# Kernel optimization log

Measured on AMD Instinct MI355X. Metric: run time of the kernel, lower is better.

The kernel has to match this reference:

```python
import jax, jax.numpy as jnp
import numpy as np

B, DV, DT, H, G, E = 4096, 1024, 1024, 1024, 4096, 8
D = DV + DT  # fused dim = 2048


def setup_inputs() -> dict:
    key = jax.random.key(0)
    ks = jax.random.split(key, 8)
    s = 0.02
    return {
        "vision_cls": jax.random.normal(ks[0], (B, DV), jnp.float32),
        "text_cls": jax.random.normal(ks[1], (B, DT), jnp.float32),
        "W1_imm": jax.random.normal(ks[2], (E, D, H), jnp.float32) * s,
        "b1_imm": jnp.zeros((E, H), jnp.float32),
        "W2_imm": jax.random.normal(ks[3], (E, H, 1), jnp.float32) * s,
        "b2_imm": jnp.zeros((E, 1), jnp.float32),
        "W1_gene": jax.random.normal(ks[4], (E, D, H), jnp.float32) * s,
        "b1_gene": jnp.zeros((E, H), jnp.float32),
        "W2_gene": jax.random.normal(ks[5], (E, H, G), jnp.float32) * s,
        "b2_gene": jnp.zeros((E, G), jnp.float32),
        "organ_idx": jax.random.randint(ks[6], (B,), 0, E, jnp.int32),
    }


def reference(vision_cls, text_cls, W1_imm, b1_imm, W2_imm, b2_imm,
              W1_gene, b1_gene, W2_gene, b2_gene, organ_idx):
    # fused features [B, D]
    fused = jnp.concatenate([vision_cls, text_cls], axis=-1)
    # Dense MoE reference: run every organ head on the full batch, then
    # select each sample's routed output (same math as the per-group
    # gather -> MLP -> scatter in the original; dropout is eval-mode identity).
    h_i = jax.nn.relu(jnp.einsum('bd,edh->ebh', fused, W1_imm) + b1_imm[:, None, :])
    imm_all = jnp.einsum('ebh,eh->eb', h_i, W2_imm[:, :, 0]) + b2_imm[:, :1]  # [E,B]
    h_g = jax.nn.relu(jnp.einsum('bd,edh->ebh', fused, W1_gene) + b1_gene[:, None, :])
    gene_all = jnp.einsum('ebh,ehg->ebg', h_g, W2_gene) + b2_gene[:, None, :]  # [E,B,G]
    bidx = jnp.arange(fused.shape[0])
    immune = imm_all[organ_idx, bidx]      # [B]
    gene = gene_all[organ_idx, bidx]       # [B,G] (uniform gene_dim -> no padding needed)
    return immune, gene, vision_cls, text_cls
```

## Files before the change

### kernel.cpp

```cpp
#include <hip/hip_runtime.h>


#define B_N 4096
#define DV  1024
#define DD  2048
#define HH  1024
#define GG  4096
#define EE  8
#define BM  128
#define MAXRB 40
#define PERM_N (MAXRB * BM)

typedef __bf16 bf16x8 __attribute__((ext_vector_type(8)));
typedef float f32x4 __attribute__((ext_vector_type(4)));
typedef unsigned short u16x4v __attribute__((ext_vector_type(4)));
typedef unsigned short u16x8v __attribute__((ext_vector_type(8)));

#define H_CNT 0
#define H_FIL 8
#define H_OFF 16
#define H_NRB 24
#define H_BLK 32

static __device__ __forceinline__ unsigned short f2bf(float f) {
  return __builtin_bit_cast(unsigned short, (__bf16)f);
}
static __device__ __forceinline__ float bf2f(unsigned short s) {
  return __builtin_bit_cast(float, (unsigned)s << 16);
}
static __device__ __forceinline__ void gload16(const void* g, void* l) {
  __builtin_amdgcn_global_load_lds(
      (const __attribute__((address_space(1))) unsigned int*)g,
      (__attribute__((address_space(3))) unsigned int*)l, 16, 0, 0);
}

__global__ __launch_bounds__(1024) void routing(const int* __restrict__ organ,
                                                int* __restrict__ hdr,
                                                int* __restrict__ perm) {
  __shared__ int cnt[EE], fil[EE], off[EE];
  const int tid = threadIdx.x;
  if (tid < EE) { cnt[tid] = 0; fil[tid] = 0; }
  __syncthreads();
#pragma unroll
  for (int i = 0; i < 4; ++i) atomicAdd(&cnt[organ[tid + (i << 10)]], 1);
#pragma unroll
  for (int i = 0; i < 5; ++i) perm[tid + (i << 10)] = -1;
  __syncthreads();
  if (tid == 0) {
    int acc = 0;
    for (int e = 0; e < EE; ++e) {
      off[e] = acc;
      hdr[H_OFF + e] = acc;
      hdr[H_CNT + e] = cnt[e];
      int nb = (cnt[e] + BM - 1) >> 7;
      int rb0 = acc >> 7;
      for (int i = 0; i < nb; ++i) hdr[H_BLK + rb0 + i] = e;
      acc += nb << 7;
    }
    hdr[H_NRB] = acc >> 7;
  }
  __syncthreads();
#pragma unroll
  for (int i = 0; i < 4; ++i) {
    int b = tid + (i << 10);
    int e = organ[b];
    int slot = off[e] + atomicAdd(&fil[e], 1);
    perm[slot] = b;
  }
}

__global__ __launch_bounds__(256) void k_A(
    const float* __restrict__ vis, const float* __restrict__ txt,
    const int* __restrict__ hdr, const int* __restrict__ perm,
    unsigned short* __restrict__ Abuf) {
  const int bx = blockIdx.x;
  const int nr = hdr[H_NRB] << 7;
  const int tid = threadIdx.x;
  const int c = tid << 3;
  const float* srcbase = (c < DV) ? vis : txt;
  const int cc = (c < DV) ? c : c - DV;
#pragma unroll
  for (int p = 0; p < 4; ++p) {
    int r = (bx << 2) + p;
    if (r >= nr) return;
    int smp = perm[r];
    u16x8v v;
    if (smp >= 0) {
      const float* src = srcbase + (size_t)smp * 1024 + cc;
      float4 a = *(const float4*)src, b = *(const float4*)(src + 4);
      v[0] = f2bf(a.x); v[1] = f2bf(a.y); v[2] = f2bf(a.z); v[3] = f2bf(a.w);
      v[4] = f2bf(b.x); v[5] = f2bf(b.y); v[6] = f2bf(b.z); v[7] = f2bf(b.w);
    } else {
#pragma unroll
      for (int i = 0; i < 8; ++i) v[i] = 0;
    }
    *(u16x8v*)&Abuf[(size_t)r * DD + c] = v;
  }
}

static __device__ __forceinline__ void copy_body(
    int bx, const float4* __restrict__ v, const float4* __restrict__ t,
    float4* __restrict__ ov, float4* __restrict__ ot) {
  const int n4 = B_N * DV / 4;
  for (int i = bx * 256 + (int)threadIdx.x; i < n4; i += 1024 * 256) {
    ov[i] = v[i];
    ot[i] = t[i];
  }
}

template <int KDIM, int NST>
static __device__ __forceinline__ void gemm_core(
    const unsigned short* __restrict__ Aseg,
    const float* __restrict__ Bglob,
    unsigned short* smem, f32x4 (&acc)[4][4]) {
  const int tid = threadIdx.x;
  const int lane = tid & 63;
  const int wr = ((tid >> 6) >> 1) << 6, wc = ((tid >> 6) & 1) << 6;
  const int lr = lane & 15;
  const int arow = tid >> 2;
  const int kq_src = (((tid & 3) ^ ((arow >> 1) & 3)) << 3);
  const int wbase = (tid & 192) << 3;
  const int bn4 = (tid & 31) << 2;
  const int bk4 = (tid >> 5) << 2;
  constexpr int NT = KDIM / 32;

  float4 bvE[4], bvO[4];

  auto issueA = [&](int buf, int k0) {
    unsigned short* d = smem + (buf << 12) + wbase;
    gload16(Aseg + (size_t)arow * KDIM + k0 + kq_src, d);
    gload16(Aseg + (size_t)(64 + arow) * KDIM + k0 + kq_src, d + 2048);
  };
  auto issueB = [&](float4 (&bv)[4], int k0) {
    const float* p = Bglob + (size_t)(k0 + bk4) * NST + bn4;
#pragma unroll
    for (int i = 0; i < 4; ++i) bv[i] = *(const float4*)(p + (size_t)i * NST);
  };
  auto writeB = [&](int buf, float4 (&bv)[4]) {
    const float* f0 = (const float*)&bv[0];
    const float* f1 = (const float*)&bv[1];
    const float* f2 = (const float*)&bv[2];
    const float* f3 = (const float*)&bv[3];
#pragma unroll
    for (int j = 0; j < 4; ++j) {
      const int n = bn4 + j;
      const int s3 = (n ^ (n >> 3)) & 7;
      u16x4v w;
      w[0] = f2bf(f0[j]); w[1] = f2bf(f1[j]);
      w[2] = f2bf(f2[j]); w[3] = f2bf(f3[j]);
      *(u16x4v*)(smem + 16384 + (buf << 12) + (n << 5) + ((((bk4 >> 2)) ^ s3) << 2)) = w;
    }
  };
  auto compute = [&](int ab, int bb) {
    bf16x8 af[4], bfr[4];
#pragma unroll
    for (int m = 0; m < 4; ++m) {
      const int r = wr + m * 16 + lr;
      const int cs = ((lane >> 4) ^ ((r >> 1) & 3)) << 3;
      af[m] = *(const bf16x8*)&smem[(ab << 12) + r * 32 + cs];
    }
#pragma unroll
    for (int n = 0; n < 4; ++n) {
      const int fr = wc + n * 16 + lr;
      const int s3 = (fr ^ (fr >> 3)) & 7;
      const unsigned short* row = smem + 16384 + (bb << 12) + (fr << 5);
      const int g = (lane >> 4) << 1;
      union { unsigned long long q[2]; bf16x8 v; } u;
      u.q[0] = *(const unsigned long long*)(row + ((g ^ s3) << 2));
      u.q[1] = *(const unsigned long long*)(row + (((g + 1) ^ s3) << 2));
      bfr[n] = u.v;
    }
#pragma unroll
    for (int m = 0; m < 4; ++m)
#pragma unroll
      for (int n = 0; n < 4; ++n)
        acc[m][n] = __builtin_amdgcn_mfma_f32_16x16x32_bf16(af[m], bfr[n], acc[m][n], 0, 0, 0);
  };

  auto phase = [&](int t, float4 (&bvIss)[4], float4 (&bvWr)[4]) {
    if (t + 3 < NT) issueA((t + 3) & 3, (t + 3) << 5);
    __builtin_amdgcn_sched_barrier(0);
    if (t + 2 < NT) issueB(bvIss, (t + 2) << 5);
    __builtin_amdgcn_sched_barrier(0);
    compute(t & 3, t & 1);
    if (t + 1 < NT) writeB((t + 1) & 1, bvWr);
    asm volatile("s_waitcnt lgkmcnt(0)" ::: "memory");
    __builtin_amdgcn_s_barrier();
    __builtin_amdgcn_sched_barrier(0);
  };

  issueA(0, 0);
  __builtin_amdgcn_sched_barrier(0);
  issueB(bvE, 0);
  writeB(0, bvE);
  issueA(1, 1 << 5);
  __builtin_amdgcn_sched_barrier(0);
  issueA(2, 2 << 5);
  __builtin_amdgcn_sched_barrier(0);
  issueB(bvO, 1 << 5);
  asm volatile("s_waitcnt lgkmcnt(0)" ::: "memory");
  __builtin_amdgcn_s_barrier();
  __builtin_amdgcn_sched_barrier(0);

  for (int t = 0; t < NT; t += 2) {
    phase(t, bvE, bvO);
    phase(t + 1, bvO, bvE);
  }
}

#define G_L1 (MAXRB * 16)
__global__ __launch_bounds__(256) void k_L1(
    const unsigned short* __restrict__ Abuf, const float* __restrict__ W1i,
    const float* __restrict__ W1g, const float* __restrict__ b1i,
    const float* __restrict__ b1g, const int* __restrict__ hdr,
    unsigned short* __restrict__ H1, unsigned short* __restrict__ H2,
    const float4* __restrict__ vis4, const float4* __restrict__ txt4,
    float4* __restrict__ ov, float4* __restrict__ ot) {
  __shared__ __align__(16) unsigned short smem[24576];
  int bx = blockIdx.x;
  if (bx >= G_L1) { copy_body(bx - G_L1, vis4, txt4, ov, ot); return; }
  const int id = (bx & 7) * (G_L1 >> 3) + (bx >> 3);
  const int rb = id % MAXRB;
  if (rb >= hdr[H_NRB]) return;
  const int sub = id / MAXRB, head = sub >> 3, cb = (sub & 7) << 7;
  const int e = hdr[H_BLK + rb];
  const float* Bglob = (head ? W1g : W1i) + (size_t)e * DD * HH + cb;
  const float* bias = (head ? b1g : b1i) + e * HH;
  unsigned short* Hout = head ? H2 : H1;
  const int tid = threadIdx.x;
  const int lane = tid & 63, wave = tid >> 6;
  const int wr = (wave >> 1) << 6, wc = (wave & 1) << 6;
  const int lr = lane & 15;

  f32x4 acc[4][4];
#pragma unroll
  for (int m = 0; m < 4; ++m)
#pragma unroll
    for (int n = 0; n < 4; ++n) acc[m][n] = (f32x4){0.f, 0.f, 0.f, 0.f};

  gemm_core<DD, HH>(Abuf + (size_t)rb * BM * DD, Bglob, smem, acc);
  __syncthreads();

  const int r0l = wr + ((lane >> 4) << 2);
#pragma unroll
  for (int n = 0; n < 4; ++n) {
    const int col = wc + n * 16 + lr;
    const float bv = bias[cb + col];
#pragma unroll
    for (int m = 0; m < 4; ++m)
#pragma unroll
      for (int v = 0; v < 4; ++v) {
        int row = r0l + m * 16 + v;
        float x = acc[m][n][v] + bv;
        x = x > 0.f ? x : 0.f;
        smem[((row << 7) + col) ^ ((row & 7) << 3)] = f2bf(x);
      }
  }
  __syncthreads();
#pragma unroll
  for (int c = 0; c < 8; ++c) {
    int q = c * 256 + tid;
    int row = q >> 4, ch = q & 15;
    int off = ((row << 7) + (ch << 3)) ^ ((row & 7) << 3);
    u16x8v val = *(const u16x8v*)&smem[off];
    *(u16x8v*)&Hout[(size_t)(rb * BM + row) * HH + cb + (ch << 3)] = val;
  }
}

static __device__ __forceinline__ void immune_body(
    int bx, const int* __restrict__ hdr, const int* __restrict__ perm,
    const unsigned short* __restrict__ H1, const float* __restrict__ W2,
    const float* __restrict__ b2, float* __restrict__ out) {
  const int nrb = hdr[H_NRB];
  const int r = bx * 4 + (threadIdx.x >> 6);
  if (r >= nrb * BM) return;
  const int b = perm[r];
  if (b < 0) return;
  const int e = hdr[H_BLK + (r >> 7)];
  const int lane = threadIdx.x & 63;
  const unsigned short* h = H1 + (size_t)r * HH + lane * 16;
  const float* w = W2 + (size_t)e * HH + lane * 16;
  float s = 0.f;
#pragma unroll
  for (int i = 0; i < 16; ++i) s += bf2f(h[i]) * w[i];
#pragma unroll
  for (int off = 32; off >= 1; off >>= 1) s += __shfl_xor(s, off, 64);
  if (lane == 0) out[b] = s + b2[e];
}

#define G_L2 (MAXRB * 32)
__global__ __launch_bounds__(256) void k_L2(
    const unsigned short* __restrict__ H2buf, const float* __restrict__ W2g,
    const float* __restrict__ b2g, const int* __restrict__ hdr,
    const int* __restrict__ perm, float* __restrict__ outg,
    const unsigned short* __restrict__ H1, const float* __restrict__ W2i,
    const float* __restrict__ b2i, float* __restrict__ outi) {
  __shared__ __align__(16) unsigned short smem[24576];
  int bx = blockIdx.x;
  if (bx >= G_L2) {
    immune_body(bx - G_L2, hdr, perm, H1, W2i, b2i, outi);
    return;
  }
  const int id = (bx & 7) * (G_L2 >> 3) + (bx >> 3);
  const int rb = id % MAXRB;
  if (rb >= hdr[H_NRB]) return;
  const int cb = (id / MAXRB) << 7;
  const int e = hdr[H_BLK + rb];
  const float* Bglob = W2g + (size_t)e * HH * GG + cb;
  const int tid = threadIdx.x;
  const int lane = tid & 63, wave = tid >> 6;
  const int wr = (wave >> 1) << 6, wc = (wave & 1) << 6;
  const int lr = lane & 15;

  f32x4 acc[4][4];
#pragma unroll
  for (int m = 0; m < 4; ++m)
#pragma unroll
    for (int n = 0; n < 4; ++n) acc[m][n] = (f32x4){0.f, 0.f, 0.f, 0.f};

  gemm_core<HH, GG>(H2buf + (size_t)rb * BM * HH, Bglob, smem, acc);
  __syncthreads();

  const int r0l = wr + ((lane >> 4) << 2);
#pragma unroll
  for (int n = 0; n < 4; ++n) {
    const int col = wc + n * 16 + lr;
    const float bv = b2g[e * GG + cb + col];
#pragma unroll
    for (int m = 0; m < 4; ++m)
#pragma unroll
      for (int v = 0; v < 4; ++v) {
        int row = r0l + m * 16 + v;
        smem[((row << 7) + col) ^ ((row & 7) << 3)] = f2bf(acc[m][n][v] + bv);
      }
  }
  __syncthreads();
#pragma unroll
  for (int c = 0; c < 8; ++c) {
    int q = c * 256 + tid;
    int row = q >> 4, ch = q & 15;
    int sm = perm[rb * BM + row];
    if (sm < 0) continue;
    int off = ((row << 7) + (ch << 3)) ^ ((row & 7) << 3);
    u16x8v val = *(const u16x8v*)&smem[off];
    float4 f0, f1;
    f0.x = bf2f(val[0]); f0.y = bf2f(val[1]); f0.z = bf2f(val[2]); f0.w = bf2f(val[3]);
    f1.x = bf2f(val[4]); f1.y = bf2f(val[5]); f1.z = bf2f(val[6]); f1.w = bf2f(val[7]);
    float* dst = outg + (size_t)sm * GG + cb + (ch << 3);
    *(float4*)dst = f0;
    *(float4*)(dst + 4) = f1;
  }
}

extern "C" void kernel_launch(void* const* d_in, const int* in_sizes, int n_in,
                              void* d_out, int out_size, void* d_ws, size_t ws_size,
                              hipStream_t stream) {
  (void)in_sizes; (void)n_in; (void)out_size; (void)ws_size;
  const float* vis = (const float*)d_in[0];
  const float* txt = (const float*)d_in[1];
  const float* W1i = (const float*)d_in[2];
  const float* b1i = (const float*)d_in[3];
  const float* W2i = (const float*)d_in[4];
  const float* b2i = (const float*)d_in[5];
  const float* W1g = (const float*)d_in[6];
  const float* b1g = (const float*)d_in[7];
  const float* W2g = (const float*)d_in[8];
  const float* b2g = (const float*)d_in[9];
  const int* organ = (const int*)d_in[10];

  float* out_imm = (float*)d_out;
  float* out_gene = out_imm + B_N;
  float* out_vis = out_gene + (size_t)B_N * GG;
  float* out_txt = out_vis + (size_t)B_N * DV;

  int* hdr = (int*)d_ws;
  int* perm = hdr + 128;

  const size_t OFF_ABUF = 32768;
  const size_t OFF_H1 = OFF_ABUF + (size_t)PERM_N * DD * 2;
  const size_t OFF_H2 = OFF_H1 + (size_t)PERM_N * HH * 2;
  unsigned short* Abuf = (unsigned short*)((char*)d_ws + OFF_ABUF);
  unsigned short* H1 = (unsigned short*)((char*)d_ws + OFF_H1);
  unsigned short* H2 = (unsigned short*)((char*)d_ws + OFF_H2);

  routing<<<1, 1024, 0, stream>>>(organ, hdr, perm);
  k_A<<<PERM_N / 4, 256, 0, stream>>>(vis, txt, hdr, perm, Abuf);
  k_L1<<<G_L1 + 1024, 256, 0, stream>>>(Abuf, W1i, W1g, b1i, b1g, hdr, H1, H2,
                                        (const float4*)vis, (const float4*)txt,
                                        (float4*)out_vis, (float4*)out_txt);
  k_L2<<<G_L2 + PERM_N / 4, 256, 0, stream>>>(H2, W2g, b2g, hdr, perm, out_gene,
                                              H1, W2i, b2i, out_imm);
}
```

Baseline: 250.3 us.

## Shrink A-buffer ring to three stages and halve L1 tile width

```diff
diff --git a/kernel.cpp b/kernel.cpp
--- a/kernel.cpp
+++ b/kernel.cpp
@@ -108,62 +108,74 @@
   }
 }
 
-template <int KDIM, int NST>
-static __device__ __forceinline__ void gemm_core(
+template <int KDIM, int NST, int NB>
+static __device__ __forceinline__ void gemm_core3(
     const unsigned short* __restrict__ Aseg,
     const float* __restrict__ Bglob,
-    unsigned short* smem, f32x4 (&acc)[4][4]) {
+    unsigned short* smem, f32x4 (&acc)[4][NB]) {
   const int tid = threadIdx.x;
   const int lane = tid & 63;
-  const int wr = ((tid >> 6) >> 1) << 6, wc = ((tid >> 6) & 1) << 6;
+  const int wr = ((tid >> 6) >> 1) << 6;
+  const int wc = ((tid >> 6) & 1) * (NB * 16);
   const int lr = lane & 15;
   const int arow = tid >> 2;
   const int kq_src = (((tid & 3) ^ ((arow >> 1) & 3)) << 3);
   const int wbase = (tid & 192) << 3;
-  const int bn4 = (tid & 31) << 2;
-  const int bk4 = (tid >> 5) << 2;
+  const int cg = tid & (8 * NB - 1);
+  const int bn4 = cg << 2;
+  const int kr = (tid / (8 * NB)) * NB;
   constexpr int NT = KDIM / 32;
-
-  float4 bvE[4], bvO[4];
-
-  auto issueA = [&](int buf, int k0) {
-    unsigned short* d = smem + (buf << 12) + wbase;
+  constexpr int BSZ = NB * 32 * 32;
+  const int s3w = (bn4 ^ (bn4 >> 3)) & 7;
+
+  float4 bvE[NB], bvO[NB];
+  (void)s3w;
+
+  auto issueA = [&](int ab, int k0) {
+    unsigned short* d = smem + ab * 4096 + wbase;
     gload16(Aseg + (size_t)arow * KDIM + k0 + kq_src, d);
     gload16(Aseg + (size_t)(64 + arow) * KDIM + k0 + kq_src, d + 2048);
   };
-  auto issueB = [&](float4 (&bv)[4], int k0) {
-    const float* p = Bglob + (size_t)(k0 + bk4) * NST + bn4;
-#pragma unroll
-    for (int i = 0; i < 4; ++i) bv[i] = *(const float4*)(p + (size_t)i * NST);
+  auto issueB = [&](float4 (&bv)[NB], int k0) {
+    const float* p = Bglob + (size_t)(k0 + kr) * NST + bn4;
+#pragma unroll
+    for (int i = 0; i < NB; ++i) bv[i] = *(const float4*)(p + (size_t)i * NST);
   };
-  auto writeB = [&](int buf, float4 (&bv)[4]) {
-    const float* f0 = (const float*)&bv[0];
-    const float* f1 = (const float*)&bv[1];
-    const float* f2 = (const float*)&bv[2];
-    const float* f3 = (const float*)&bv[3];
+  auto writeB = [&](int bb, float4 (&bv)[NB]) {
+    unsigned short* base = smem + 12288 + bb * BSZ;
 #pragma unroll
     for (int j = 0; j < 4; ++j) {
       const int n = bn4 + j;
       const int s3 = (n ^ (n >> 3)) & 7;
-      u16x4v w;
-      w[0] = f2bf(f0[j]); w[1] = f2bf(f1[j]);
-      w[2] = f2bf(f2[j]); w[3] = f2bf(f3[j]);
-      *(u16x4v*)(smem + 16384 + (buf << 12) + (n << 5) + ((((bk4 >> 2)) ^ s3) << 2)) = w;
+      unsigned short* row = base + (n << 5);
+      if constexpr (NB == 4) {
+        u16x4v w;
+        w[0] = f2bf(((const float*)&bv[0])[j]);
+        w[1] = f2bf(((const float*)&bv[1])[j]);
+        w[2] = f2bf(((const float*)&bv[2])[j]);
+        w[3] = f2bf(((const float*)&bv[3])[j]);
+        *(u16x4v*)(row + (((kr >> 2) ^ s3) << 2)) = w;
+      } else {
+        unsigned lo = f2bf(((const float*)&bv[0])[j]);
+        unsigned hi = f2bf(((const float*)&bv[1])[j]);
+        *(unsigned*)(row + ((((kr >> 2) ^ s3) << 2) | (kr & 2))) =
+            lo | (hi << 16);
+      }
     }
   };
   auto compute = [&](int ab, int bb) {
-    bf16x8 af[4], bfr[4];
+    bf16x8 af[4], bfr[NB];
 #pragma unroll
     for (int m = 0; m < 4; ++m) {
       const int r = wr + m * 16 + lr;
       const int cs = ((lane >> 4) ^ ((r >> 1) & 3)) << 3;
-      af[m] = *(const bf16x8*)&smem[(ab << 12) + r * 32 + cs];
+      af[m] = *(const bf16x8*)&smem[ab * 4096 + r * 32 + cs];
     }
 #pragma unroll
-    for (int n = 0; n < 4; ++n) {
+    for (int n = 0; n < NB; ++n) {
       const int fr = wc + n * 16 + lr;
       const int s3 = (fr ^ (fr >> 3)) & 7;
-      const unsigned short* row = smem + 16384 + (bb << 12) + (fr << 5);
+      const unsigned short* row = smem + 12288 + bb * BSZ + (fr << 5);
       const int g = (lane >> 4) << 1;
       union { unsigned long long q[2]; bf16x8 v; } u;
       u.q[0] = *(const unsigned long long*)(row + ((g ^ s3) << 2));
@@ -173,20 +185,8 @@
 #pragma unroll
     for (int m = 0; m < 4; ++m)
 #pragma unroll
-      for (int n = 0; n < 4; ++n)
+      for (int n = 0; n < NB; ++n)
         acc[m][n] = __builtin_amdgcn_mfma_f32_16x16x32_bf16(af[m], bfr[n], acc[m][n], 0, 0, 0);
-  };
-
-  auto phase = [&](int t, float4 (&bvIss)[4], float4 (&bvWr)[4]) {
-    if (t + 3 < NT) issueA((t + 3) & 3, (t + 3) << 5);
-    __builtin_amdgcn_sched_barrier(0);
-    if (t + 2 < NT) issueB(bvIss, (t + 2) << 5);
-    __builtin_amdgcn_sched_barrier(0);
-    compute(t & 3, t & 1);
-    if (t + 1 < NT) writeB((t + 1) & 1, bvWr);
-    asm volatile("s_waitcnt lgkmcnt(0)" ::: "memory");
-    __builtin_amdgcn_s_barrier();
-    __builtin_amdgcn_sched_barrier(0);
   };
 
   issueA(0, 0);
@@ -195,55 +195,72 @@
   writeB(0, bvE);
   issueA(1, 1 << 5);
   __builtin_amdgcn_sched_barrier(0);
-  issueA(2, 2 << 5);
-  __builtin_amdgcn_sched_barrier(0);
   issueB(bvO, 1 << 5);
   asm volatile("s_waitcnt lgkmcnt(0)" ::: "memory");
   __builtin_amdgcn_s_barrier();
   __builtin_amdgcn_sched_barrier(0);
 
+  auto phase = [&](int t, int abI, int abC, float4 (&bvIss)[NB],
+                   float4 (&bvWr)[NB], int bbW, int bbC) {
+    if (t + 2 < NT) issueA(abI, (t + 2) << 5);
+    __builtin_amdgcn_sched_barrier(0);
+    if (t + 2 < NT) issueB(bvIss, (t + 2) << 5);
+    __builtin_amdgcn_sched_barrier(0);
+    compute(abC, bbC);
+    if (t + 1 < NT) writeB(bbW, bvWr);
+    asm volatile("s_waitcnt lgkmcnt(0)" ::: "memory");
+    __builtin_amdgcn_s_barrier();
+    __builtin_amdgcn_sched_barrier(0);
+  };
+
+  int abI = 2, abC = 0;
   for (int t = 0; t < NT; t += 2) {
-    phase(t, bvE, bvO);
-    phase(t + 1, bvO, bvE);
-  }
-}
-
-#define G_L1 (MAXRB * 16)
-__global__ __launch_bounds__(256) void k_L1(
+    phase(t, abI, abC, bvE, bvO, 1, 0);
+    abI = (abI == 2) ? 0 : abI + 1;
+    abC = (abC == 2) ? 0 : abC + 1;
+    phase(t + 1, abI, abC, bvO, bvE, 0, 1);
+    abI = (abI == 2) ? 0 : abI + 1;
+    abC = (abC == 2) ? 0 : abC + 1;
+  }
+}
+
+#define G_L1 (MAXRB * 32)
+__global__ __launch_bounds__(256, 5) void k_L1(
     const unsigned short* __restrict__ Abuf, const float* __restrict__ W1i,
     const float* __restrict__ W1g, const float* __restrict__ b1i,
     const float* __restrict__ b1g, const int* __restrict__ hdr,
     unsigned short* __restrict__ H1, unsigned short* __restrict__ H2,
     const float4* __restrict__ vis4, const float4* __restrict__ txt4,
     float4* __restrict__ ov, float4* __restrict__ ot) {
-  __shared__ __align__(16) unsigned short smem[24576];
+  __shared__ __align__(16) unsigned short smem[16384];
   int bx = blockIdx.x;
   if (bx >= G_L1) { copy_body(bx - G_L1, vis4, txt4, ov, ot); return; }
   const int id = (bx & 7) * (G_L1 >> 3) + (bx >> 3);
   const int rb = id % MAXRB;
   if (rb >= hdr[H_NRB]) return;
-  const int sub = id / MAXRB, head = sub >> 3, cb = (sub & 7) << 7;
+  const int sub = id / MAXRB;
+  const int head = sub >> 4, cb = (sub & 15) << 6;
   const int e = hdr[H_BLK + rb];
   const float* Bglob = (head ? W1g : W1i) + (size_t)e * DD * HH + cb;
   const float* bias = (head ? b1g : b1i) + e * HH;
   unsigned short* Hout = head ? H2 : H1;
   const int tid = threadIdx.x;
   const int lane = tid & 63, wave = tid >> 6;
-  const int wr = (wave >> 1) << 6, wc = (wave & 1) << 6;
+  const int wr = (wave >> 1) << 6, wc = (wave & 1) << 5;
   const int lr = lane & 15;
 
-  f32x4 acc[4][4];
+  f32x4 acc[4][2];
 #pragma unroll
   for (int m = 0; m < 4; ++m)
 #pragma unroll
-    for (int n = 0; n < 4; ++n) acc[m][n] = (f32x4){0.f, 0.f, 0.f, 0.f};
-
-  gemm_core<DD, HH>(Abuf + (size_t)rb * BM * DD, Bglob, smem, acc);
+    for (int n = 0; n < 2; ++n) acc[m][n] = (f32x4){0.f, 0.f, 0.f, 0.f};
+
+  gemm_core3<DD, HH, 2>(Abuf + (size_t)rb * BM * DD, Bglob, smem, acc);
   __syncthreads();
 
   const int r0l = wr + ((lane >> 4) << 2);
 #pragma unroll
-  for (int n = 0; n < 4; ++n) {
+  for (int n = 0; n < 2; ++n) {
     const int col = wc + n * 16 + lr;
     const float bv = bias[cb + col];
 #pragma unroll
@@ -253,15 +270,15 @@
         int row = r0l + m * 16 + v;
         float x = acc[m][n][v] + bv;
         x = x > 0.f ? x : 0.f;
-        smem[((row << 7) + col) ^ ((row & 7) << 3)] = f2bf(x);
+        smem[((row << 6) + col) ^ ((row & 7) << 3)] = f2bf(x);
       }
   }
   __syncthreads();
 #pragma unroll
-  for (int c = 0; c < 8; ++c) {
+  for (int c = 0; c < 4; ++c) {
     int q = c * 256 + tid;
-    int row = q >> 4, ch = q & 15;
-    int off = ((row << 7) + (ch << 3)) ^ ((row & 7) << 3);
+    int row = q >> 3, ch = q & 7;
+    int off = ((row << 6) + (ch << 3)) ^ ((row & 7) << 3);
     u16x8v val = *(const u16x8v*)&smem[off];
     *(u16x8v*)&Hout[(size_t)(rb * BM + row) * HH + cb + (ch << 3)] = val;
   }
@@ -289,13 +306,13 @@
 }
 
 #define G_L2 (MAXRB * 32)
-__global__ __launch_bounds__(256) void k_L2(
+__global__ __launch_bounds__(256, 4) void k_L2(
     const unsigned short* __restrict__ H2buf, const float* __restrict__ W2g,
     const float* __restrict__ b2g, const int* __restrict__ hdr,
     const int* __restrict__ perm, float* __restrict__ outg,
     const unsigned short* __restrict__ H1, const float* __restrict__ W2i,
     const float* __restrict__ b2i, float* __restrict__ outi) {
-  __shared__ __align__(16) unsigned short smem[24576];
+  __shared__ __align__(16) unsigned short smem[20480];
   int bx = blockIdx.x;
   if (bx >= G_L2) {
     immune_body(bx - G_L2, hdr, perm, H1, W2i, b2i, outi);
@@ -318,7 +335,7 @@
 #pragma unroll
     for (int n = 0; n < 4; ++n) acc[m][n] = (f32x4){0.f, 0.f, 0.f, 0.f};
 
-  gemm_core<HH, GG>(H2buf + (size_t)rb * BM * HH, Bglob, smem, acc);
+  gemm_core3<HH, GG, 4>(H2buf + (size_t)rb * BM * HH, Bglob, smem, acc);
   __syncthreads();
 
   const int r0l = wr + ((lane >> 4) << 2);
```

After: 337.5 us. 34.9% more time.

## Pre-convert weights to transposed bf16 and load B tiles directly in GEMMs

Applied to the files above, without the earlier changes.

```diff
diff --git a/kernel.cpp b/kernel.cpp
--- a/kernel.cpp
+++ b/kernel.cpp
@@ -13,7 +13,6 @@
 
 typedef __bf16 bf16x8 __attribute__((ext_vector_type(8)));
 typedef float f32x4 __attribute__((ext_vector_type(4)));
-typedef unsigned short u16x4v __attribute__((ext_vector_type(4)));
 typedef unsigned short u16x8v __attribute__((ext_vector_type(8)));
 
 #define H_CNT 0
@@ -69,11 +68,38 @@
   }
 }
 
-__global__ __launch_bounds__(256) void k_A(
-    const float* __restrict__ vis, const float* __restrict__ txt,
+static __device__ __forceinline__ void wcvt_body(
+    const float* __restrict__ in, unsigned short* __restrict__ out,
+    int K, int N, int bx, unsigned short* ls) {
+  const int nn = N >> 6, nk = K >> 6;
+  const int e = bx / (nk * nn);
+  int rem = bx - e * nk * nn;
+  const int K0 = (rem / nn) << 6, N0 = (rem % nn) << 6;
+  const size_t ein = (size_t)e * K * N;
+  const int tid = threadIdx.x;
+  const int kr = tid >> 4, n0 = (tid & 15) << 2;
+#pragma unroll
+  for (int p = 0; p < 4; ++p) {
+    int k = (p << 4) + kr;
+    float4 f = *(const float4*)&in[ein + (size_t)(K0 + k) * N + N0 + n0];
+    ls[(n0 + 0) * 72 + k] = f2bf(f.x);
+    ls[(n0 + 1) * 72 + k] = f2bf(f.y);
+    ls[(n0 + 2) * 72 + k] = f2bf(f.z);
+    ls[(n0 + 3) * 72 + k] = f2bf(f.w);
+  }
+  __syncthreads();
+  const int n = tid >> 2, kc = (tid & 3) << 4;
+  u16x8v a = *(const u16x8v*)&ls[n * 72 + kc];
+  u16x8v b = *(const u16x8v*)&ls[n * 72 + kc + 8];
+  size_t o = (size_t)e * N * K + (size_t)(N0 + n) * K + K0 + kc;
+  *(u16x8v*)&out[o] = a;
+  *(u16x8v*)&out[o + 8] = b;
+}
+
+static __device__ __forceinline__ void abuild_body(
+    int bx, const float* __restrict__ vis, const float* __restrict__ txt,
     const int* __restrict__ hdr, const int* __restrict__ perm,
     unsigned short* __restrict__ Abuf) {
-  const int bx = blockIdx.x;
   const int nr = hdr[H_NRB] << 7;
   const int tid = threadIdx.x;
   const int c = tid << 3;
@@ -108,48 +134,41 @@
   }
 }
 
-template <int KDIM, int NST>
-static __device__ __forceinline__ void gemm_core(
+template <int KDIM>
+static __device__ __forceinline__ void gemm_bb(
     const unsigned short* __restrict__ Aseg,
-    const float* __restrict__ Bglob,
+    const unsigned short* __restrict__ Bseg,
     unsigned short* smem, f32x4 (&acc)[4][4]) {
   const int tid = threadIdx.x;
   const int lane = tid & 63;
   const int wr = ((tid >> 6) >> 1) << 6, wc = ((tid >> 6) & 1) << 6;
   const int lr = lane & 15;
   const int arow = tid >> 2;
-  const int kq_src = (((tid & 3) ^ ((arow >> 1) & 3)) << 3);
+  const int kq = (((tid & 3) ^ ((arow >> 1) & 3)) << 3);
   const int wbase = (tid & 192) << 3;
-  const int bn4 = (tid & 31) << 2;
-  const int bk4 = (tid >> 5) << 2;
+  const int bn = tid & 127;
+  const int bc0 = (tid >> 7) << 1;
+  const int bs = (bn >> 1) & 3;
+  const int bslot0 = ((bc0 ^ bs) << 3);
+  const int bslot1 = (((bc0 + 1) ^ bs) << 3);
   constexpr int NT = KDIM / 32;
 
-  float4 bvE[4], bvO[4];
-
-  auto issueA = [&](int buf, int k0) {
-    unsigned short* d = smem + (buf << 12) + wbase;
-    gload16(Aseg + (size_t)arow * KDIM + k0 + kq_src, d);
-    gload16(Aseg + (size_t)(64 + arow) * KDIM + k0 + kq_src, d + 2048);
+  u16x8v bvE[2], bvO[2];
+
+  auto issueA = [&](int ab, int k0) {
+    unsigned short* d = smem + ab * 4096 + wbase;
+    gload16(Aseg + (size_t)arow * KDIM + k0 + kq, d);
+    gload16(Aseg + (size_t)(64 + arow) * KDIM + k0 + kq, d + 2048);
   };
-  auto issueB = [&](float4 (&bv)[4], int k0) {
-    const float* p = Bglob + (size_t)(k0 + bk4) * NST + bn4;
-#pragma unroll
-    for (int i = 0; i < 4; ++i) bv[i] = *(const float4*)(p + (size_t)i * NST);
+  auto issueB = [&](u16x8v (&bv)[2], int k0) {
+    const unsigned short* p = Bseg + (size_t)bn * KDIM + k0 + (bc0 << 3);
+    bv[0] = *(const u16x8v*)p;
+    bv[1] = *(const u16x8v*)(p + 8);
   };
-  auto writeB = [&](int buf, float4 (&bv)[4]) {
-    const float* f0 = (const float*)&bv[0];
-    const float* f1 = (const float*)&bv[1];
-    const float* f2 = (const float*)&bv[2];
-    const float* f3 = (const float*)&bv[3];
-#pragma unroll
-    for (int j = 0; j < 4; ++j) {
-      const int n = bn4 + j;
-      const int s3 = (n ^ (n >> 3)) & 7;
-      u16x4v w;
-      w[0] = f2bf(f0[j]); w[1] = f2bf(f1[j]);
-      w[2] = f2bf(f2[j]); w[3] = f2bf(f3[j]);
-      *(u16x4v*)(smem + 16384 + (buf << 12) + (n << 5) + ((((bk4 >> 2)) ^ s3) << 2)) = w;
-    }
+  auto writeB = [&](int bb, u16x8v (&bv)[2]) {
+    unsigned short* row = smem + 12288 + bb * 4096 + (bn << 5);
+    *(u16x8v*)(row + bslot0) = bv[0];
+    *(u16x8v*)(row + bslot1) = bv[1];
   };
   auto compute = [&](int ab, int bb) {
     bf16x8 af[4], bfr[4];
@@ -157,18 +176,13 @@
     for (int m = 0; m < 4; ++m) {
       const int r = wr + m * 16 + lr;
       const int cs = ((lane >> 4) ^ ((r >> 1) & 3)) << 3;
-      af[m] = *(const bf16x8*)&smem[(ab << 12) + r * 32 + cs];
+      af[m] = *(const bf16x8*)&smem[ab * 4096 + r * 32 + cs];
     }
 #pragma unroll
     for (int n = 0; n < 4; ++n) {
       const int fr = wc + n * 16 + lr;
-      const int s3 = (fr ^ (fr >> 3)) & 7;
-      const unsigned short* row = smem + 16384 + (bb << 12) + (fr << 5);
-      const int g = (lane >> 4) << 1;
-      union { unsigned long long q[2]; bf16x8 v; } u;
-      u.q[0] = *(const unsigned long long*)(row + ((g ^ s3) << 2));
-      u.q[1] = *(const unsigned long long*)(row + (((g + 1) ^ s3) << 2));
-      bfr[n] = u.v;
+      const int cs = ((lane >> 4) ^ ((fr >> 1) & 3)) << 3;
+      bfr[n] = *(const bf16x8*)&smem[12288 + bb * 4096 + fr * 32 + cs];
     }
 #pragma unroll
     for (int m = 0; m < 4; ++m)
@@ -177,54 +191,84 @@
         acc[m][n] = __builtin_amdgcn_mfma_f32_16x16x32_bf16(af[m], bfr[n], acc[m][n], 0, 0, 0);
   };
 
-  auto phase = [&](int t, float4 (&bvIss)[4], float4 (&bvWr)[4]) {
-    if (t + 3 < NT) issueA((t + 3) & 3, (t + 3) << 5);
+  issueA(0, 0);
+  __builtin_amdgcn_sched_barrier(0);
+  issueB(bvE, 0);
+  writeB(0, bvE);
+  issueA(1, 32);
+  __builtin_amdgcn_sched_barrier(0);
+  issueB(bvO, 32);
+  asm volatile("s_waitcnt lgkmcnt(0)" ::: "memory");
+  __builtin_amdgcn_s_barrier();
+  __builtin_amdgcn_sched_barrier(0);
+
+  auto phase = [&](int t, int abI, int abC, u16x8v (&bvIss)[2],
+                   u16x8v (&bvWr)[2], int bbW, int bbC) {
+    if (t + 2 < NT) issueA(abI, (t + 2) << 5);
     __builtin_amdgcn_sched_barrier(0);
     if (t + 2 < NT) issueB(bvIss, (t + 2) << 5);
     __builtin_amdgcn_sched_barrier(0);
-    compute(t & 3, t & 1);
-    if (t + 1 < NT) writeB((t + 1) & 1, bvWr);
+    compute(abC, bbC);
+    if (t + 1 < NT) writeB(bbW, bvWr);
     asm volatile("s_waitcnt lgkmcnt(0)" ::: "memory");
     __builtin_amdgcn_s_barrier();
     __builtin_amdgcn_sched_barrier(0);
   };
 
-  issueA(0, 0);
-  __builtin_amdgcn_sched_barrier(0);
-  issueB(bvE, 0);
-  writeB(0, bvE);
-  issueA(1, 1 << 5);
-  __builtin_amdgcn_sched_barrier(0);
-  issueA(2, 2 << 5);
-  __builtin_amdgcn_sched_barrier(0);
-  issueB(bvO, 1 << 5);
-  asm volatile("s_waitcnt lgkmcnt(0)" ::: "memory");
-  __builtin_amdgcn_s_barrier();
-  __builtin_amdgcn_sched_barrier(0);
-
+  int abI = 2, abC = 0;
   for (int t = 0; t < NT; t += 2) {
-    phase(t, bvE, bvO);
-    phase(t + 1, bvO, bvE);
-  }
-}
-
-#define G_L1 (MAXRB * 16)
-__global__ __launch_bounds__(256) void k_L1(
-    const unsigned short* __restrict__ Abuf, const float* __restrict__ W1i,
-    const float* __restrict__ W1g, const float* __restrict__ b1i,
-    const float* __restrict__ b1g, const int* __restrict__ hdr,
-    unsigned short* __restrict__ H1, unsigned short* __restrict__ H2,
-    const float4* __restrict__ vis4, const float4* __restrict__ txt4,
-    float4* __restrict__ ov, float4* __restrict__ ot) {
-  __shared__ __align__(16) unsigned short smem[24576];
+    phase(t, abI, abC, bvE, bvO, 1, 0);
+    abI = (abI == 2) ? 0 : abI + 1;
+    abC = (abC == 2) ? 0 : abC + 1;
+    phase(t + 1, abI, abC, bvO, bvE, 0, 1);
+    abI = (abI == 2) ? 0 : abI + 1;
+    abC = (abC == 2) ? 0 : abC + 1;
+  }
+}
+
+#define G_CVT1 (EE * (DD >> 6) * (HH >> 6))
+#define G_AB   (PERM_N / 4)
+__global__ __launch_bounds__(256) void k_prep(
+    const float* __restrict__ W1i, const float* __restrict__ W1g,
+    unsigned short* __restrict__ W1i_t, unsigned short* __restrict__ W1g_t,
+    const float* __restrict__ vis, const float* __restrict__ txt,
+    const int* __restrict__ hdr, const int* __restrict__ perm,
+    unsigned short* __restrict__ Abuf) {
+  __shared__ __align__(16) unsigned short sm[64 * 72];
   int bx = blockIdx.x;
-  if (bx >= G_L1) { copy_body(bx - G_L1, vis4, txt4, ov, ot); return; }
-  const int id = (bx & 7) * (G_L1 >> 3) + (bx >> 3);
+  if (bx < G_CVT1) { wcvt_body(W1i, W1i_t, DD, HH, bx, sm); return; }
+  bx -= G_CVT1;
+  if (bx < G_CVT1) { wcvt_body(W1g, W1g_t, DD, HH, bx, sm); return; }
+  bx -= G_CVT1;
+  abuild_body(bx, vis, txt, hdr, perm, Abuf);
+}
+
+#define G_G1   (MAXRB * 16)
+#define G_CVT2 (EE * (HH >> 6) * (GG >> 6))
+#define G_COPY 1024
+__global__ __launch_bounds__(256) void k_main1(
+    const unsigned short* __restrict__ Abuf,
+    const unsigned short* __restrict__ W1i_t, const unsigned short* __restrict__ W1g_t,
+    const float* __restrict__ b1i, const float* __restrict__ b1g,
+    const int* __restrict__ hdr, unsigned short* __restrict__ H1,
+    unsigned short* __restrict__ H2, const float* __restrict__ W2g,
+    unsigned short* __restrict__ W2g_t, const float4* __restrict__ vis4,
+    const float4* __restrict__ txt4, float4* __restrict__ ov,
+    float4* __restrict__ ot) {
+  __shared__ __align__(16) unsigned short smem[20480];
+  int bx = blockIdx.x;
+  if (bx >= G_G1) {
+    bx -= G_G1;
+    if (bx < G_CVT2) { wcvt_body(W2g, W2g_t, HH, GG, bx, smem); return; }
+    copy_body(bx - G_CVT2, vis4, txt4, ov, ot);
+    return;
+  }
+  const int id = (bx & 7) * (G_G1 >> 3) + (bx >> 3);
   const int rb = id % MAXRB;
   if (rb >= hdr[H_NRB]) return;
   const int sub = id / MAXRB, head = sub >> 3, cb = (sub & 7) << 7;
   const int e = hdr[H_BLK + rb];
-  const float* Bglob = (head ? W1g : W1i) + (size_t)e * DD * HH + cb;
+  const unsigned short* Wt = (head ? W1g_t : W1i_t) + (size_t)e * HH * DD + (size_t)cb * DD;
   const float* bias = (head ? b1g : b1i) + e * HH;
   unsigned short* Hout = head ? H2 : H1;
   const int tid = threadIdx.x;
@@ -238,7 +282,7 @@
 #pragma unroll
     for (int n = 0; n < 4; ++n) acc[m][n] = (f32x4){0.f, 0.f, 0.f, 0.f};
 
-  gemm_core<DD, HH>(Abuf + (size_t)rb * BM * DD, Bglob, smem, acc);
+  gemm_bb<DD>(Abuf + (size_t)rb * BM * DD, Wt, smem, acc);
   __syncthreads();
 
   const int r0l = wr + ((lane >> 4) << 2);
@@ -288,25 +332,26 @@
   if (lane == 0) out[b] = s + b2[e];
 }
 
-#define G_L2 (MAXRB * 32)
-__global__ __launch_bounds__(256) void k_L2(
-    const unsigned short* __restrict__ H2buf, const float* __restrict__ W2g,
-    const float* __restrict__ b2g, const int* __restrict__ hdr,
-    const int* __restrict__ perm, float* __restrict__ outg,
-    const unsigned short* __restrict__ H1, const float* __restrict__ W2i,
-    const float* __restrict__ b2i, float* __restrict__ outi) {
-  __shared__ __align__(16) unsigned short smem[24576];
+#define G_G2 (MAXRB * 32)
+__global__ __launch_bounds__(256) void k_main2(
+    const unsigned short* __restrict__ H2buf,
+    const unsigned short* __restrict__ W2g_t, const float* __restrict__ b2g,
+    const int* __restrict__ hdr, const int* __restrict__ perm,
+    float* __restrict__ outg, const unsigned short* __restrict__ H1,
+    const float* __restrict__ W2i, const float* __restrict__ b2i,
+    float* __restrict__ outi) {
+  __shared__ __align__(16) unsigned short smem[20480];
   int bx = blockIdx.x;
-  if (bx >= G_L2) {
-    immune_body(bx - G_L2, hdr, perm, H1, W2i, b2i, outi);
+  if (bx >= G_G2) {
+    immune_body(bx - G_G2, hdr, perm, H1, W2i, b2i, outi);
     return;
   }
-  const int id = (bx & 7) * (G_L2 >> 3) + (bx >> 3);
+  const int id = (bx & 7) * (G_G2 >> 3) + (bx >> 3);
   const int rb = id % MAXRB;
   if (rb >= hdr[H_NRB]) return;
   const int cb = (id / MAXRB) << 7;
   const int e = hdr[H_BLK + rb];
-  const float* Bglob = W2g + (size_t)e * HH * GG + cb;
+  const unsigned short* Wt = W2g_t + (size_t)e * GG * HH + (size_t)cb * HH;
   const int tid = threadIdx.x;
   const int lane = tid & 63, wave = tid >> 6;
   const int wr = (wave >> 1) << 6, wc = (wave & 1) << 6;
@@ -318,7 +363,7 @@
 #pragma unroll
     for (int n = 0; n < 4; ++n) acc[m][n] = (f32x4){0.f, 0.f, 0.f, 0.f};
 
-  gemm_core<HH, GG>(H2buf + (size_t)rb * BM * HH, Bglob, smem, acc);
+  gemm_bb<HH>(H2buf + (size_t)rb * BM * HH, Wt, smem, acc);
   __syncthreads();
 
   const int r0l = wr + ((lane >> 4) << 2);
@@ -379,15 +424,24 @@
   const size_t OFF_ABUF = 32768;
   const size_t OFF_H1 = OFF_ABUF + (size_t)PERM_N * DD * 2;
   const size_t OFF_H2 = OFF_H1 + (size_t)PERM_N * HH * 2;
+  const size_t OFF_W1I = OFF_H2 + (size_t)PERM_N * HH * 2;
+  const size_t OFF_W1G = OFF_W1I + (size_t)EE * HH * DD * 2;
+  const size_t OFF_W2G = OFF_W1G + (size_t)EE * HH * DD * 2;
   unsigned short* Abuf = (unsigned short*)((char*)d_ws + OFF_ABUF);
   unsigned short* H1 = (unsigned short*)((char*)d_ws + OFF_H1);
   unsigned short* H2 = (unsigned short*)((char*)d_ws + OFF_H2);
+  unsigned short* W1i_t = (unsigned short*)((char*)d_ws + OFF_W1I);
+  unsigned short* W1g_t = (unsigned short*)((char*)d_ws + OFF_W1G);
+  unsigned short* W2g_t = (unsigned short*)((char*)d_ws + OFF_W2G);
 
   routing<<<1, 1024, 0, stream>>>(organ, hdr, perm);
-  k_A<<<PERM_N / 4, 256, 0, stream>>>(vis, txt, hdr, perm, Abuf);
-  k_L1<<<G_L1 + 1024, 256, 0, stream>>>(Abuf, W1i, W1g, b1i, b1g, hdr, H1, H2,
-                                        (const float4*)vis, (const float4*)txt,
-                                        (float4*)out_vis, (float4*)out_txt);
-  k_L2<<<G_L2 + PERM_N / 4, 256, 0, stream>>>(H2, W2g, b2g, hdr, perm, out_gene,
-                                              H1, W2i, b2i, out_imm);
-}
+  k_prep<<<G_CVT1 * 2 + G_AB, 256, 0, stream>>>(W1i, W1g, W1i_t, W1g_t, vis,
+                                                txt, hdr, perm, Abuf);
+  k_main1<<<G_G1 + G_CVT2 + G_COPY, 256, 0, stream>>>(
+      Abuf, W1i_t, W1g_t, b1i, b1g, hdr, H1, H2, W2g, W2g_t,
+      (const float4*)vis, (const float4*)txt, (float4*)out_vis,
+      (float4*)out_txt);
+  k_main2<<<G_G2 + PERM_N / 4, 256, 0, stream>>>(H2, W2g_t, b2g, hdr, perm,
+                                                 out_gene, H1, W2i, b2i,
+                                                 out_imm);
+}
```

Result: no change. 252.7 us (+1.0%).
